# Performance work log

Hardware: AMD Instinct MI355X
Metric: run time of the kernel (lower is better)

Reference implementation:

```python
import jax, jax.numpy as jnp
import numpy as np

L, S, D = 2, 2048, 2048          # layers, seq_len, model dim
H, KVH, HD = 16, 4, 128          # heads, kv heads, head_dim (scale 128**0.5 is hardcoded in source)
F = 8192                         # ffn hidden
EPS = 1e-5
THETA = 500000.0                 # Llama-3 rope base


def setup_inputs() -> dict:
    key = jax.random.key(0)
    ks = jax.random.split(key, 9)
    sc = 0.02
    x = jax.random.normal(ks[0], (S, D), jnp.float32)
    inv_freq = 1.0 / (THETA ** (jnp.arange(0, HD, 2, dtype=jnp.float32) / HD))  # [HD/2]
    ang = jnp.arange(S, dtype=jnp.float32)[:, None] * inv_freq[None, :]         # [S, HD/2]
    w = lambda k, shape: jax.random.normal(k, shape, jnp.float32) * sc
    return {
        "token_embeddings_unnormal": x,
        "freqs_cos": jnp.cos(ang),
        "freqs_sin": jnp.sin(ang),
        "attn_norm_w": jnp.ones((L, D), jnp.float32),
        "wq": w(ks[1], (L, D, D)),
        "wk": w(ks[2], (L, KVH * HD, D)),
        "wv": w(ks[3], (L, KVH * HD, D)),
        "wo": w(ks[4], (L, D, D)),
        "ffn_norm_w": jnp.ones((L, D), jnp.float32),
        "w1": w(ks[5], (L, F, D)),
        "w2": w(ks[6], (L, D, F)),
        "w3": w(ks[7], (L, F, D)),
    }


def _rms_norm(x, w):
    # x * rsqrt(mean(x^2) + eps) * w  (matches source exactly)
    return x * jax.lax.rsqrt(jnp.mean(x * x, axis=-1, keepdims=True) + EPS) * w


def _rope(t, cos, sin):
    # t: [S, h, HD]; complex rotation of consecutive pairs by freqs_cis
    tp = t.reshape(t.shape[0], t.shape[1], HD // 2, 2)
    t0, t1 = tp[..., 0], tp[..., 1]
    c, s = cos[:, None, :], sin[:, None, :]
    return jnp.stack([t0 * c - t1 * s, t0 * s + t1 * c], axis=-1).reshape(t.shape)


def reference(token_embeddings_unnormal, freqs_cos, freqs_sin, attn_norm_w,
              wq, wk, wv, wo, ffn_norm_w, w1, w2, w3):
    x = token_embeddings_unnormal
    scale = 1.0 / np.sqrt(128.0)
    causal = jnp.tril(jnp.ones((S, S), bool))
    for l in range(L):
        h = _rms_norm(x, attn_norm_w[l])
        # batched per-head projections (source loops over heads; same math)
        q = jnp.einsum('sd,hed->she', h, wq[l].reshape(H, HD, D))
        k = jnp.einsum('sd,hed->she', h, wk[l].reshape(KVH, HD, D))
        v = jnp.einsum('sd,hed->she', h, wv[l].reshape(KVH, HD, D))
        q = _rope(q, freqs_cos, freqs_sin)
        k = _rope(k, freqs_cos, freqs_sin)
        # GQA: head `i` uses kv head i // 4
        k = jnp.repeat(k, H // KVH, axis=1)
        v = jnp.repeat(v, H // KVH, axis=1)
        scores = jnp.einsum('she,the->hst', q, k) * scale
        scores = jnp.where(causal[None], scores, -jnp.inf)
        probs = jax.nn.softmax(scores, axis=-1).astype(jnp.bfloat16).astype(jnp.float32)
        attn = jnp.einsum('hst,the->she', probs, v).reshape(S, H * HD)
        x = x + attn @ wo[l].T
        hf = _rms_norm(x, ffn_norm_w[l])
        x = x + (jax.nn.silu(hf @ w1[l].T) * (hf @ w3[l].T)) @ w2[l].T
    return x
```

## Files before the change

kernel.cpp:

```cpp
#include <hip/hip_runtime.h>

#define SLEN 2048
#define DM   2048
#define NH   16
#define NKVH 4
#define HD   128
#define KVD  512
#define FF   8192
#define NLAYER 2
#define EPSV 1e-5f

typedef unsigned short bhalf;
typedef __attribute__((__ext_vector_type__(8))) __bf16 bf16x8;
typedef __attribute__((__ext_vector_type__(4))) float f32x4;

__device__ __forceinline__ float b2f(bhalf u) {
  union { unsigned int i; float f; } v; v.i = ((unsigned int)u) << 16; return v.f;
}
__device__ __forceinline__ bhalf f2b(float f) {
  unsigned int x = __float_as_uint(f);
  return (bhalf)((x + 0x7fffu + ((x >> 16) & 1u)) >> 16);
}

typedef __attribute__((address_space(1))) const void gas_cvoid;
typedef __attribute__((address_space(3))) void las_void;
__device__ __forceinline__ void gload16(const void* g, void* l) {
  __builtin_amdgcn_global_load_lds((gas_cvoid*)g, (las_void*)l, 16, 0, 0);
}
__device__ __forceinline__ f32x4 mfma16(bf16x8 a, bf16x8 b, f32x4 c) {
  return __builtin_amdgcn_mfma_f32_16x16x32_bf16(a, b, c, 0, 0, 0);
}

__global__ __launch_bounds__(256)
void cvt_f32_bf16(const float* __restrict__ in, bhalf* __restrict__ out, size_t n) {
  size_t i = ((size_t)blockIdx.x * 256 + threadIdx.x) * 8;
  const size_t stride = (size_t)gridDim.x * 256 * 8;
  for (; i < n; i += stride) {
    float4 a = *(const float4*)(in + i);
    float4 b = *(const float4*)(in + i + 4);
    int4 o; bhalf* t = (bhalf*)&o;
    t[0]=f2b(a.x); t[1]=f2b(a.y); t[2]=f2b(a.z); t[3]=f2b(a.w);
    t[4]=f2b(b.x); t[5]=f2b(b.y); t[6]=f2b(b.z); t[7]=f2b(b.w);
    *(int4*)(out + i) = o;
  }
}

__global__ __launch_bounds__(256)
void rmsnorm_k(const float* __restrict__ x, const float* __restrict__ w,
               bhalf* __restrict__ out) {
  const int row = blockIdx.x;
  const int tid = threadIdx.x;
  const float4* xr = (const float4*)(x + (size_t)row * DM);
  float4 a = xr[tid*2], b = xr[tid*2 + 1];
  float ss = a.x*a.x + a.y*a.y + a.z*a.z + a.w*a.w
           + b.x*b.x + b.y*b.y + b.z*b.z + b.w*b.w;
  #pragma unroll
  for (int off = 32; off > 0; off >>= 1) ss += __shfl_down(ss, off);
  __shared__ float red[5];
  const int wv = tid >> 6, l = tid & 63;
  if (l == 0) red[wv] = ss;
  __syncthreads();
  if (tid == 0) red[4] = rsqrtf((red[0]+red[1]+red[2]+red[3]) * (1.0f/DM) + EPSV);
  __syncthreads();
  const float rs = red[4];
  const float* wp = w + tid*8;
  float vals[8] = {a.x,a.y,a.z,a.w,b.x,b.y,b.z,b.w};
  int4 o; bhalf* t = (bhalf*)&o;
  #pragma unroll
  for (int j = 0; j < 8; ++j) t[j] = f2b(vals[j] * rs * wp[j]);
  *(int4*)(out + (size_t)row*DM + tid*8) = o;
}

__global__ __launch_bounds__(256)
void rope_k(bhalf* __restrict__ t, const float* __restrict__ c,
            const float* __restrict__ s, int nheads) {
  const int idx = blockIdx.x * 256 + threadIdx.x;
  const int j  = idx & 63;
  const int hh = (idx >> 6) % nheads;
  const int sp = idx / (nheads * 64);
  const float cv = c[sp*64 + j], sv = s[sp*64 + j];
  unsigned int* p = (unsigned int*)(t + ((size_t)sp*nheads + hh)*HD + 2*j);
  const unsigned int pv = *p;
  const float t0 = b2f((bhalf)(pv & 0xffffu)), t1 = b2f((bhalf)(pv >> 16));
  const float o0 = t0*cv - t1*sv, o1 = t0*sv + t1*cv;
  *p = (unsigned int)f2b(o0) | ((unsigned int)f2b(o1) << 16);
}

template<int EPI>
__global__ __launch_bounds__(256, 2)
void gemm_bt(const bhalf* __restrict__ A, const bhalf* __restrict__ B,
             const int N, const int K,
             const bhalf* __restrict__ gate,
             float* __restrict__ outf, bhalf* __restrict__ outb) {
  __shared__ bhalf As[128*32];
  __shared__ bhalf Bs[128*32];
  const int tid = threadIdx.x;
  const int w = tid >> 6, l = tid & 63;
  const int l15 = l & 15, lg = l >> 4;
  const int ntn = N >> 7;
  const int nblocks = gridDim.x;
  const int qq = nblocks >> 3, rr = nblocks & 7;
  const int xcd = blockIdx.x & 7, loc = blockIdx.x >> 3;
  const int swz = (xcd < rr) ? (xcd*(qq+1) + loc) : (rr*(qq+1) + (xcd-rr)*qq + loc);
  const size_t m0 = (size_t)(swz / ntn) << 7;
  const size_t n0 = (size_t)(swz % ntn) << 7;
  f32x4 acc[4][4] = {};
  const int wr = w >> 1, wc = w & 1;
  const int stgrow = l >> 2;
  const int stgcol = (l & 3) << 3;
  const int nk = K >> 5;
  for (int kt = 0; kt < nk; ++kt) {
    const int k0 = kt << 5;
    #pragma unroll
    for (int it = 0; it < 2; ++it) {
      const int c = it*4 + w;
      const int row = c*16 + stgrow;
      gload16(&A[(m0 + row)*K + k0 + stgcol], &As[c*512]);
      gload16(&B[(n0 + row)*K + k0 + stgcol], &Bs[c*512]);
    }
    __syncthreads();
    bf16x8 af[4], bfr[4];
    #pragma unroll
    for (int m = 0; m < 4; ++m)
      af[m] = *(const bf16x8*)&As[(wr*64 + m*16 + l15)*32 + lg*8];
    #pragma unroll
    for (int n = 0; n < 4; ++n)
      bfr[n] = *(const bf16x8*)&Bs[(wc*64 + n*16 + l15)*32 + lg*8];
    #pragma unroll
    for (int m = 0; m < 4; ++m)
      #pragma unroll
      for (int n = 0; n < 4; ++n)
        acc[m][n] = mfma16(af[m], bfr[n], acc[m][n]);
    __syncthreads();
  }
  #pragma unroll
  for (int m = 0; m < 4; ++m) {
    const size_t row = m0 + wr*64 + m*16 + lg*4;
    #pragma unroll
    for (int n = 0; n < 4; ++n) {
      const size_t col = n0 + wc*64 + n*16 + l15;
      #pragma unroll
      for (int r2 = 0; r2 < 4; ++r2) {
        const size_t idx = (row + r2)*(size_t)N + col;
        const float v = acc[m][n][r2];
        if constexpr (EPI == 1) {
          outb[idx] = f2b(v);
        } else if constexpr (EPI == 2) {
          outf[idx] += v;
        } else {
          const float g = b2f(gate[idx]);
          const float si = g / (1.0f + __expf(-g));
          outb[idx] = f2b(si * v);
        }
      }
    }
  }
}

__global__ __launch_bounds__(256, 2)
void attn_k(const bhalf* __restrict__ qb, const bhalf* __restrict__ kb,
            const bhalf* __restrict__ vb, bhalf* __restrict__ ob) {
  __shared__ bhalf Ks[64][144];
  __shared__ bhalf Vt[128][80];
  __shared__ bhalf Ps[4][16][80];
  const int h  = blockIdx.x >> 5;
  const int qt = blockIdx.x & 31;
  const int kvh = h >> 2;
  const int tid = threadIdx.x;
  const int w = tid >> 6, l = tid & 63;
  const int l15 = l & 15, lg = l >> 4;
  const int q0 = qt << 6;

  bf16x8 qf[4];
  {
    const bhalf* qrow = qb + (size_t)(q0 + w*16 + l15)*DM + h*HD + lg*8;
    #pragma unroll
    for (int kc = 0; kc < 4; ++kc) qf[kc] = *(const bf16x8*)(qrow + kc*32);
  }
  float m_r[4] = {-3e38f,-3e38f,-3e38f,-3e38f};
  float l_r[4] = {0.f,0.f,0.f,0.f};
  f32x4 acc_o[8] = {};
  const float scale = 0.08838834764831845f;
  const int nt = qt + 1;
  for (int t = 0; t < nt; ++t) {
    const int k0 = t << 6;
    __syncthreads();
    #pragma unroll
    for (int it = 0; it < 4; ++it) {
      const int e = it*256 + tid;
      const int row = e >> 4;
      const int col = (e & 15) << 3;
      *(int4*)&Ks[row][col] =
          *(const int4*)(kb + (size_t)(k0 + row)*KVD + kvh*HD + col);
    }
    {
      const int d = tid & 127, g = tid >> 7;
      const bhalf* vp = vb + (size_t)(k0 + g*32)*KVD + kvh*HD + d;
      #pragma unroll
      for (int kk8 = 0; kk8 < 4; ++kk8) {
        int4 o; bhalf* tt = (bhalf*)&o;
        #pragma unroll
        for (int j2 = 0; j2 < 8; ++j2) tt[j2] = vp[(size_t)(kk8*8 + j2)*KVD];
        *(int4*)&Vt[d][g*32 + kk8*8] = o;
      }
    }
    __syncthreads();
    f32x4 sa[4] = {};
    #pragma unroll
    for (int kc = 0; kc < 4; ++kc)
      #pragma unroll
      for (int n = 0; n < 4; ++n) {
        bf16x8 kf = *(const bf16x8*)&Ks[n*16 + l15][kc*32 + lg*8];
        sa[n] = mfma16(qf[kc], kf, sa[n]);
      }
    const bool masked = (t == qt);
    #pragma unroll
    for (int r = 0; r < 4; ++r) {
      const int qg = q0 + w*16 + lg*4 + r;
      float sv[4];
      #pragma unroll
      for (int n = 0; n < 4; ++n) {
        float s = sa[n][r] * scale;
        if (masked && (k0 + n*16 + l15 > qg)) s = -3e38f;
        sv[n] = s;
      }
      float tm = fmaxf(fmaxf(sv[0], sv[1]), fmaxf(sv[2], sv[3]));
      tm = fmaxf(tm, __shfl_xor(tm, 1));
      tm = fmaxf(tm, __shfl_xor(tm, 2));
      tm = fmaxf(tm, __shfl_xor(tm, 4));
      tm = fmaxf(tm, __shfl_xor(tm, 8));
      const float mn = fmaxf(m_r[r], tm);
      const float alpha = __expf(m_r[r] - mn);
      float pv[4], psum = 0.f;
      #pragma unroll
      for (int n = 0; n < 4; ++n) { pv[n] = __expf(sv[n] - mn); psum += pv[n]; }
      psum += __shfl_xor(psum, 1);
      psum += __shfl_xor(psum, 2);
      psum += __shfl_xor(psum, 4);
      psum += __shfl_xor(psum, 8);
      l_r[r] = l_r[r]*alpha + psum;
      m_r[r] = mn;
      #pragma unroll
      for (int n2 = 0; n2 < 8; ++n2) acc_o[n2][r] *= alpha;
      #pragma unroll
      for (int n = 0; n < 4; ++n) Ps[w][lg*4 + r][n*16 + l15] = f2b(pv[n]);
    }
    #pragma unroll
    for (int kk = 0; kk < 2; ++kk) {
      bf16x8 pa = *(const bf16x8*)&Ps[w][l15][kk*32 + lg*8];
      #pragma unroll
      for (int n2 = 0; n2 < 8; ++n2) {
        bf16x8 vf = *(const bf16x8*)&Vt[n2*16 + l15][kk*32 + lg*8];
        acc_o[n2] = mfma16(pa, vf, acc_o[n2]);
      }
    }
  }
  #pragma unroll
  for (int r = 0; r < 4; ++r) {
    const float inv = 1.0f / l_r[r];
    bhalf* orow = ob + (size_t)(q0 + w*16 + lg*4 + r)*DM + h*HD;
    #pragma unroll
    for (int n2 = 0; n2 < 8; ++n2) orow[n2*16 + l15] = f2b(acc_o[n2][r] * inv);
  }
}

extern "C" void kernel_launch(void* const* d_in, const int* in_sizes, int n_in,
                              void* d_out, int out_size, void* d_ws, size_t ws_size,
                              hipStream_t stream) {
  (void)in_sizes; (void)n_in; (void)out_size; (void)ws_size;
  const float* x_in = (const float*)d_in[0];
  const float* fcos = (const float*)d_in[1];
  const float* fsin = (const float*)d_in[2];
  const float* anw  = (const float*)d_in[3];
  const float* wq   = (const float*)d_in[4];
  const float* wk   = (const float*)d_in[5];
  const float* wv   = (const float*)d_in[6];
  const float* wo   = (const float*)d_in[7];
  const float* fnw  = (const float*)d_in[8];
  const float* w1   = (const float*)d_in[9];
  const float* w2   = (const float*)d_in[10];
  const float* w3   = (const float*)d_in[11];
  float* x = (float*)d_out;

  char* p = (char*)d_ws;
  auto carve = [&](size_t elems) {
    bhalf* r = (bhalf*)p; p += ((elems*2 + 255) & ~(size_t)255); return r;
  };
  bhalf* wq_b = carve((size_t)NLAYER*DM*DM);
  bhalf* wk_b = carve((size_t)NLAYER*KVD*DM);
  bhalf* wv_b = carve((size_t)NLAYER*KVD*DM);
  bhalf* wo_b = carve((size_t)NLAYER*DM*DM);
  bhalf* w1_b = carve((size_t)NLAYER*FF*DM);
  bhalf* w2_b = carve((size_t)NLAYER*DM*FF);
  bhalf* w3_b = carve((size_t)NLAYER*FF*DM);
  bhalf* hn   = carve((size_t)SLEN*DM);
  bhalf* qb   = carve((size_t)SLEN*DM);
  bhalf* kb   = carve((size_t)SLEN*KVD);
  bhalf* vb   = carve((size_t)SLEN*KVD);
  bhalf* ab   = carve((size_t)SLEN*DM);
  bhalf* g1   = carve((size_t)SLEN*FF);

  hipMemcpyAsync(x, x_in, (size_t)SLEN*DM*sizeof(float),
                 hipMemcpyDeviceToDevice, stream);

  cvt_f32_bf16<<<2048,256,0,stream>>>(wq, wq_b, (size_t)NLAYER*DM*DM);
  cvt_f32_bf16<<<2048,256,0,stream>>>(wk, wk_b, (size_t)NLAYER*KVD*DM);
  cvt_f32_bf16<<<2048,256,0,stream>>>(wv, wv_b, (size_t)NLAYER*KVD*DM);
  cvt_f32_bf16<<<2048,256,0,stream>>>(wo, wo_b, (size_t)NLAYER*DM*DM);
  cvt_f32_bf16<<<2048,256,0,stream>>>(w1, w1_b, (size_t)NLAYER*FF*DM);
  cvt_f32_bf16<<<2048,256,0,stream>>>(w2, w2_b, (size_t)NLAYER*DM*FF);
  cvt_f32_bf16<<<2048,256,0,stream>>>(w3, w3_b, (size_t)NLAYER*FF*DM);

  for (int l = 0; l < NLAYER; ++l) {
    rmsnorm_k<<<SLEN,256,0,stream>>>(x, anw + l*DM, hn);
    gemm_bt<1><<<256,256,0,stream>>>(hn, wq_b + (size_t)l*DM*DM,  DM,  DM, nullptr, nullptr, qb);
    gemm_bt<1><<<64, 256,0,stream>>>(hn, wk_b + (size_t)l*KVD*DM, KVD, DM, nullptr, nullptr, kb);
    gemm_bt<1><<<64, 256,0,stream>>>(hn, wv_b + (size_t)l*KVD*DM, KVD, DM, nullptr, nullptr, vb);
    rope_k<<<SLEN*NH*64/256,  256,0,stream>>>(qb, fcos, fsin, NH);
    rope_k<<<SLEN*NKVH*64/256,256,0,stream>>>(kb, fcos, fsin, NKVH);
    attn_k<<<NH*(SLEN/64),256,0,stream>>>(qb, kb, vb, ab);
    gemm_bt<2><<<256,256,0,stream>>>(ab, wo_b + (size_t)l*DM*DM, DM, DM, nullptr, x, nullptr);
    rmsnorm_k<<<SLEN,256,0,stream>>>(x, fnw + l*DM, hn);
    gemm_bt<1><<<1024,256,0,stream>>>(hn, w1_b + (size_t)l*FF*DM, FF, DM, nullptr, nullptr, g1);
    gemm_bt<3><<<1024,256,0,stream>>>(hn, w3_b + (size_t)l*FF*DM, FF, DM, g1, nullptr, g1);
    gemm_bt<2><<<256, 256,0,stream>>>(g1, w2_b + (size_t)l*DM*FF, DM, FF, nullptr, x, nullptr);
  }
}
```

Measured before the change: 1.813 ms.

## Add 256x256-tile triple-buffered GEMM with split-K atomics for FFN projections

Adds a new 512-thread GEMM kernel with 256x256 output tiles, a three-stage LDS ring buffer, XCD-aware block remapping and swizzled shared-memory reads. It replaces the FFN w1, w3 and w2 GEMMs. The down projection uses split-K by 4 with atomicAdd into the fp32 residual. The larger tiles are meant to raise arithmetic intensity and reuse, and split-K restores parallelism for the small-N w2 GEMM. In exchange the kernel holds more registers and LDS per block, and the atomics make the residual sum order nondeterministic.

```diff
diff --git a/kernel.cpp b/kernel.cpp
--- a/kernel.cpp
+++ b/kernel.cpp
@@ -157,6 +157,122 @@
   }
 }
 
+template<int EPI>
+__global__ __launch_bounds__(512, 2)
+void gemm256(const bhalf* __restrict__ A, const bhalf* __restrict__ B,
+             const int N, const int lda, const int klen,
+             const bhalf* __restrict__ gate, float* __restrict__ outf,
+             bhalf* __restrict__ outb) {
+  __shared__ __align__(16) bhalf As[3][256*32];
+  __shared__ __align__(16) bhalf Bs[3][256*32];
+  const int tid = threadIdx.x;
+  const int w = tid >> 6, l = tid & 63;
+  const int l15 = l & 15, lg = l >> 4;
+  const int rdswz = (l15 >> 1) & 3;
+  const int wr = w >> 2, wc = w & 3;
+  const int ntn = N >> 8;
+  const int nblocks = gridDim.x;
+  const int qq = nblocks >> 3, rr = nblocks & 7;
+  const int xcd = blockIdx.x & 7, loc = blockIdx.x >> 3;
+  const int sb = (xcd < rr) ? (xcd*(qq+1) + loc) : (rr*(qq+1) + (xcd-rr)*qq + loc);
+  const size_t m0 = (size_t)(sb / ntn) << 8;
+  const size_t n0 = (size_t)(sb % ntn) << 8;
+  const int k0 = blockIdx.y * klen;
+  const int nk = klen >> 5;
+  const int srow = l >> 2;
+  const int scol = ((l & 3) ^ ((l >> 3) & 3)) << 3;
+  const bhalf* Ag = A + m0 * (size_t)lda + k0;
+  const bhalf* Bg = B + n0 * (size_t)lda + k0;
+
+  auto stage = [&](int kt, int buf) {
+    #pragma unroll
+    for (int r = 0; r < 2; ++r) {
+      const int chunk = r*8 + w;
+      const size_t go = (size_t)(chunk*16 + srow)*lda + kt*32 + scol;
+      gload16(Ag + go, &As[buf][chunk*512]);
+      gload16(Bg + go, &Bs[buf][chunk*512]);
+    }
+  };
+
+  f32x4 acc[8][4] = {};
+  auto compute = [&](int cb) {
+    const bhalf* Ab = As[cb];
+    const bhalf* Bb = Bs[cb];
+    const int co = (lg ^ rdswz) << 3;
+    bf16x8 bfr[4], am[4];
+    #pragma unroll
+    for (int n = 0; n < 4; ++n)
+      bfr[n] = *(const bf16x8*)&Bb[(wc*64 + n*16 + l15)*32 + co];
+    #pragma unroll
+    for (int m = 0; m < 4; ++m)
+      am[m] = *(const bf16x8*)&Ab[(wr*128 + m*16 + l15)*32 + co];
+    __builtin_amdgcn_s_setprio(1);
+    #pragma unroll
+    for (int m = 0; m < 4; ++m)
+      #pragma unroll
+      for (int n = 0; n < 4; ++n)
+        acc[m][n] = mfma16(am[m], bfr[n], acc[m][n]);
+    __builtin_amdgcn_s_setprio(0);
+    #pragma unroll
+    for (int m = 0; m < 4; ++m)
+      am[m] = *(const bf16x8*)&Ab[(wr*128 + 64 + m*16 + l15)*32 + co];
+    __builtin_amdgcn_s_setprio(1);
+    #pragma unroll
+    for (int m = 0; m < 4; ++m)
+      #pragma unroll
+      for (int n = 0; n < 4; ++n)
+        acc[m + 4][n] = mfma16(am[m], bfr[n], acc[m + 4][n]);
+    __builtin_amdgcn_s_setprio(0);
+  };
+
+  stage(0, 0);
+  stage(1, 1);
+  asm volatile("s_waitcnt vmcnt(4)" ::: "memory");
+  __builtin_amdgcn_s_barrier();
+  asm volatile("" ::: "memory");
+
+  int cb = 0, pb = 2;
+  for (int kt = 0; kt < nk - 2; ++kt) {
+    stage(kt + 2, pb);
+    compute(cb);
+    asm volatile("s_waitcnt vmcnt(4)" ::: "memory");
+    __builtin_amdgcn_s_barrier();
+    asm volatile("" ::: "memory");
+    cb = (cb + 1 == 3) ? 0 : cb + 1;
+    pb = (pb + 1 == 3) ? 0 : pb + 1;
+  }
+  compute(cb);
+  asm volatile("s_waitcnt vmcnt(0)" ::: "memory");
+  __builtin_amdgcn_s_barrier();
+  asm volatile("" ::: "memory");
+  cb = (cb + 1 == 3) ? 0 : cb + 1;
+  compute(cb);
+
+  #pragma unroll
+  for (int m = 0; m < 8; ++m) {
+    const size_t row = m0 + wr*128 + m*16 + lg*4;
+    #pragma unroll
+    for (int n = 0; n < 4; ++n) {
+      const size_t col = n0 + wc*64 + n*16 + l15;
+      #pragma unroll
+      for (int r2 = 0; r2 < 4; ++r2) {
+        const size_t idx = (row + r2) * (size_t)N + col;
+        const float v = acc[m][n][r2];
+        if constexpr (EPI == 1) {
+          outb[idx] = f2b(v);
+        } else if constexpr (EPI == 2) {
+          outf[idx] += v;
+        } else if constexpr (EPI == 3) {
+          const float g = b2f(gate[idx]);
+          outb[idx] = f2b((g / (1.0f + __expf(-g))) * v);
+        } else {
+          atomicAdd(&outf[idx], v);
+        }
+      }
+    }
+  }
+}
+
 __global__ __launch_bounds__(256, 2)
 void attn_k(const bhalf* __restrict__ qb, const bhalf* __restrict__ kb,
             const bhalf* __restrict__ vb, bhalf* __restrict__ ob) {
@@ -321,8 +437,11 @@
     attn_k<<<NH*(SLEN/64),256,0,stream>>>(qb, kb, vb, ab);
     gemm_bt<2><<<256,256,0,stream>>>(ab, wo_b + (size_t)l*DM*DM, DM, DM, nullptr, x, nullptr);
     rmsnorm_k<<<SLEN,256,0,stream>>>(x, fnw + l*DM, hn);
-    gemm_bt<1><<<1024,256,0,stream>>>(hn, w1_b + (size_t)l*FF*DM, FF, DM, nullptr, nullptr, g1);
-    gemm_bt<3><<<1024,256,0,stream>>>(hn, w3_b + (size_t)l*FF*DM, FF, DM, g1, nullptr, g1);
-    gemm_bt<2><<<256, 256,0,stream>>>(g1, w2_b + (size_t)l*DM*FF, DM, FF, nullptr, x, nullptr);
-  }
-}
+    gemm256<1><<<dim3((SLEN/256)*(FF/256),1),512,0,stream>>>(
+        hn, w1_b + (size_t)l*FF*DM, FF, DM, DM, nullptr, nullptr, g1);
+    gemm256<3><<<dim3((SLEN/256)*(FF/256),1),512,0,stream>>>(
+        hn, w3_b + (size_t)l*FF*DM, FF, DM, DM, g1, nullptr, g1);
+    gemm256<5><<<dim3((SLEN/256)*(DM/256),4),512,0,stream>>>(
+        g1, w2_b + (size_t)l*DM*FF, DM, FF, FF/4, nullptr, x, nullptr);
+  }
+}
```

Result: faster. 1.735 ms (-4.3%).
